# Optimization experiments

Hardware: AMD Instinct MI355X
Metric: run time of the kernel (lower is better)

The kernel has to match this reference:

```python
import jax, jax.numpy as jnp
import numpy as np

N_NODES = 100000
EMB_DIM = 128
HIDDEN = 64
N_EDGES = 1600000


def setup_inputs() -> dict:
    key = jax.random.key(0)
    k_emb, k_ei, k_w1, k_b1, k_w2, k_b2 = jax.random.split(key, 6)
    node_embeddings = jax.random.normal(k_emb, (N_NODES, EMB_DIM), dtype=jnp.float32)
    edge_index = jax.random.randint(k_ei, (2, N_EDGES), 0, N_NODES, dtype=jnp.int64)
    in_dim = 2 * EMB_DIM
    # Kaiming-uniform-ish init like torch Linear
    lim1 = 1.0 / np.sqrt(in_dim)
    lim2 = 1.0 / np.sqrt(HIDDEN)
    W1 = jax.random.uniform(k_w1, (in_dim, HIDDEN), minval=-lim1, maxval=lim1, dtype=jnp.float32)
    b1 = jax.random.uniform(k_b1, (HIDDEN,), minval=-lim1, maxval=lim1, dtype=jnp.float32)
    W2 = jax.random.uniform(k_w2, (HIDDEN, 1), minval=-lim2, maxval=lim2, dtype=jnp.float32)
    b2 = jax.random.uniform(k_b2, (1,), minval=-lim2, maxval=lim2, dtype=jnp.float32)
    return {"node_embeddings": node_embeddings, "edge_index": edge_index,
            "W1": W1, "b1": b1, "W2": W2, "b2": b2}


def reference(node_embeddings, edge_index, W1, b1, W2, b2):
    # Gather source/target node embeddings per edge
    src = node_embeddings[edge_index[0]]            # [E, D]
    tgt = node_embeddings[edge_index[1]]            # [E, D]
    edge_features = jnp.concatenate([src, tgt], axis=1)  # [E, 2D]
    h = jax.nn.relu(edge_features @ W1 + b1)        # [E, H]; dropout = identity (eval)
    edge_scores = (h @ W2 + b2).squeeze(-1)         # [E]
    return edge_scores
```

## Files before the change

kernel.cpp:

```cpp
#include <hip/hip_runtime.h>
#include <hip/hip_bf16.h>

typedef float f32x4 __attribute__((ext_vector_type(4)));
typedef __bf16 bf16x8 __attribute__((ext_vector_type(8)));
typedef _Float16 f16x2 __attribute__((ext_vector_type(2)));
typedef _Float16 f16x8 __attribute__((ext_vector_type(8)));
typedef unsigned short u16;

__device__ inline u16 f2bf(float f) {
    unsigned int u = __float_as_uint(f);
    return (u16)((u + 0x7fffu + ((u >> 16) & 1u)) >> 16);
}

__device__ inline bf16x8 pack8(const float4 a, const float4 b) {
    union { u16 h[8]; bf16x8 v; } r;
    r.h[0] = f2bf(a.x); r.h[1] = f2bf(a.y); r.h[2] = f2bf(a.z); r.h[3] = f2bf(a.w);
    r.h[4] = f2bf(b.x); r.h[5] = f2bf(b.y); r.h[6] = f2bf(b.z); r.h[7] = f2bf(b.w);
    return r.v;
}

__global__ __launch_bounds__(256) void cvt_w_kernel(const float* __restrict__ W1,
                                                    u16* __restrict__ wf) {
    int i = blockIdx.x * 256 + threadIdx.x;
    if (i >= 128 * 128) return;
    int j = i & 7, fl = i >> 3;
    int lane = fl & 63, kbt = fl >> 6;
    int kb = kbt >> 3, t = kbt & 7;
    int k = kb * 32 + ((lane >> 4) & 3) * 8 + j;
    int n = t * 16 + (lane & 15);
    int krow = k + ((n >= 64) ? 128 : 0);
    wf[i] = f2bf(W1[krow * 64 + (n & 63)]);
}

__global__ __launch_bounds__(256) void uv_gemm_kernel(
    const float* __restrict__ emb, const u16* __restrict__ wf,
    _Float16* __restrict__ uv, int M) {
    __shared__ __align__(16) u16 bsh[32 * 64 * 8];

    const int tid = threadIdx.x;
    const int w = tid >> 6, lane = tid & 63, quad = lane >> 4, l15 = lane & 15;
    {
        const uint4* s = (const uint4*)wf;
        uint4* d = (uint4*)bsh;
#pragma unroll
        for (int i = 0; i < 8; ++i) d[tid + i * 256] = s[tid + i * 256];
    }
    __syncthreads();

    const int rb = blockIdx.x * 128 + w * 32;

    bf16x8 a[2][4];
#pragma unroll
    for (int m = 0; m < 2; ++m) {
        int row = rb + m * 16 + l15;
        if (row >= M) row = M - 1;
        const float* p = emb + (long)row * 128 + quad * 8;
#pragma unroll
        for (int kb = 0; kb < 4; ++kb) {
            float4 x = ((const float4*)(p + kb * 32))[0];
            float4 y = ((const float4*)(p + kb * 32))[1];
            a[m][kb] = pack8(x, y);
        }
    }

    f32x4 acc[2][8];
#pragma unroll
    for (int m = 0; m < 2; ++m)
#pragma unroll
        for (int t = 0; t < 8; ++t)
#pragma unroll
            for (int r = 0; r < 4; ++r) acc[m][t][r] = 0.0f;

#pragma unroll
    for (int kb = 0; kb < 4; ++kb)
#pragma unroll
        for (int t = 0; t < 8; ++t) {
            bf16x8 bf = *(const bf16x8*)(bsh + ((kb * 8 + t) * 64 + lane) * 8);
#pragma unroll
            for (int m = 0; m < 2; ++m)
                acc[m][t] = __builtin_amdgcn_mfma_f32_16x16x32_bf16(a[m][kb], bf,
                                                                    acc[m][t], 0, 0, 0);
        }

#pragma unroll
    for (int m = 0; m < 2; ++m)
#pragma unroll
        for (int t = 0; t < 8; ++t)
#pragma unroll
            for (int r = 0; r < 4; ++r) {
                int row = rb + m * 16 + quad * 4 + r;
                if (row < M) uv[(long)row * 128 + t * 16 + l15] = (_Float16)acc[m][t][r];
            }
}

__device__ inline f16x2 relu2(f16x2 x) {
    f16x2 r;
    r[0] = (x[0] > (_Float16)0.f) ? x[0] : (_Float16)0.f;
    r[1] = (x[1] > (_Float16)0.f) ? x[1] : (_Float16)0.f;
    return r;
}

__global__ __launch_bounds__(256, 8) void edge_score_kernel(
    const _Float16* __restrict__ uv, const int* __restrict__ idx,
    const float* __restrict__ b1, const float* __restrict__ w2,
    const float* __restrict__ b2, float* __restrict__ out, int E, int nT) {
    const int tid = threadIdx.x, w = tid >> 6, lane = tid & 63;
    const int e4 = lane >> 2, q = lane & 3;

    f16x2 b1h[8], w2h[8];
#pragma unroll
    for (int i = 0; i < 4; ++i) {
        b1h[i][0]     = (_Float16)b1[q * 8 + 2 * i];
        b1h[i][1]     = (_Float16)b1[q * 8 + 2 * i + 1];
        b1h[4 + i][0] = (_Float16)b1[32 + q * 8 + 2 * i];
        b1h[4 + i][1] = (_Float16)b1[32 + q * 8 + 2 * i + 1];
        w2h[i][0]     = (_Float16)w2[q * 8 + 2 * i];
        w2h[i][1]     = (_Float16)w2[q * 8 + 2 * i + 1];
        w2h[4 + i][0] = (_Float16)w2[32 + q * 8 + 2 * i];
        w2h[4 + i][1] = (_Float16)w2[32 + q * 8 + 2 * i + 1];
    }
    const float b2v = b2[0];

    const int gw = blockIdx.x * 4 + w, stride = gridDim.x * 4;

    auto ldidx = [&](int tile, int& s, int& t) {
        int e = tile * 16 + e4;
        if (e >= E) e = E - 1;
        s = idx[e];
        t = idx[E + e];
    };
    int src, tgt;
    ldidx(gw < nT ? gw : 0, src, tgt);

    union F8 { f16x8 v; f16x2 p[4]; };

    for (int tile = gw; tile < nT; tile += stride) {
        int nt2 = tile + stride, sn, tn;
        ldidx(nt2 < nT ? nt2 : tile, sn, tn);

        const _Float16* up = uv + (long)src * 128;
        const _Float16* vp = uv + (long)tgt * 128;
        F8 U0, U1, V0, V1;
        U0.v = *(const f16x8*)(up + q * 8);
        U1.v = *(const f16x8*)(up + 32 + q * 8);
        V0.v = *(const f16x8*)(vp + 64 + q * 8);
        V1.v = *(const f16x8*)(vp + 96 + q * 8);

        float s = 0.f;
#pragma unroll
        for (int i = 0; i < 4; ++i) {
            f16x2 h = relu2((U0.p[i] + V0.p[i]) + b1h[i]);
#if __has_builtin(__builtin_amdgcn_fdot2)
            s = __builtin_amdgcn_fdot2(h, w2h[i], s, false);
#else
            s += (float)h[0] * (float)w2h[i][0] + (float)h[1] * (float)w2h[i][1];
#endif
        }
#pragma unroll
        for (int i = 0; i < 4; ++i) {
            f16x2 h = relu2((U1.p[i] + V1.p[i]) + b1h[4 + i]);
#if __has_builtin(__builtin_amdgcn_fdot2)
            s = __builtin_amdgcn_fdot2(h, w2h[4 + i], s, false);
#else
            s += (float)h[0] * (float)w2h[4 + i][0] + (float)h[1] * (float)w2h[4 + i][1];
#endif
        }
        s += __shfl_xor(s, 1, 64);
        s += __shfl_xor(s, 2, 64);
        if (q == 0) {
            int e = tile * 16 + e4;
            if (e < E) out[e] = s + b2v;
        }
        src = sn; tgt = tn;
    }
}

extern "C" void kernel_launch(void* const* d_in, const int* in_sizes, int n_in,
                              void* d_out, int out_size, void* d_ws, size_t ws_size,
                              hipStream_t stream) {
    const float* emb_f = (const float*)d_in[0];
    const int*   idx   = (const int*)d_in[1];
    const float* W1    = (const float*)d_in[2];
    const float* b1    = (const float*)d_in[3];
    const float* W2    = (const float*)d_in[4];
    const float* b2    = (const float*)d_in[5];
    float* out = (float*)d_out;

    const int embN = in_sizes[0];
    const int M    = embN / 128;
    const int E    = in_sizes[1] / 2;

    _Float16* uv = (_Float16*)d_ws;
    u16* wf = (u16*)(uv + (long)M * 128);

    cvt_w_kernel<<<64, 256, 0, stream>>>(W1, wf);
    uv_gemm_kernel<<<(M + 127) / 128, 256, 0, stream>>>(emb_f, wf, uv, M);

    int nT = (E + 15) / 16;
    edge_score_kernel<<<2048, 256, 0, stream>>>(uv, idx, b1, W2, b2, out, E, nT);
}
```

Before: 159.8 us.

## Fuse W1 bf16 conversion into GEMM, halve rows per block, nontemporal index/output

Removes the separate weight-conversion kernel launch: each GEMM block now converts and swizzles W1 from fp32 directly into shared memory. The GEMM block handles 64 rows instead of 128, which doubles the block count and halves per-wave accumulators. The edge kernel uses nontemporal loads for edge indices and nontemporal stores for scores so this streaming data does not pollute the cache. In exchange, every block redoes the 16K-element W1 conversion with strided fp32 reads, and there are now about 1563 such blocks.

```diff
diff --git a/kernel.cpp b/kernel.cpp
--- a/kernel.cpp
+++ b/kernel.cpp
@@ -19,78 +19,62 @@
     return r.v;
 }
 
-__global__ __launch_bounds__(256) void cvt_w_kernel(const float* __restrict__ W1,
-                                                    u16* __restrict__ wf) {
-    int i = blockIdx.x * 256 + threadIdx.x;
-    if (i >= 128 * 128) return;
-    int j = i & 7, fl = i >> 3;
-    int lane = fl & 63, kbt = fl >> 6;
-    int kb = kbt >> 3, t = kbt & 7;
-    int k = kb * 32 + ((lane >> 4) & 3) * 8 + j;
-    int n = t * 16 + (lane & 15);
-    int krow = k + ((n >= 64) ? 128 : 0);
-    wf[i] = f2bf(W1[krow * 64 + (n & 63)]);
-}
-
 __global__ __launch_bounds__(256) void uv_gemm_kernel(
-    const float* __restrict__ emb, const u16* __restrict__ wf,
+    const float* __restrict__ emb, const float* __restrict__ W1,
     _Float16* __restrict__ uv, int M) {
     __shared__ __align__(16) u16 bsh[32 * 64 * 8];
 
     const int tid = threadIdx.x;
     const int w = tid >> 6, lane = tid & 63, quad = lane >> 4, l15 = lane & 15;
-    {
-        const uint4* s = (const uint4*)wf;
-        uint4* d = (uint4*)bsh;
-#pragma unroll
-        for (int i = 0; i < 8; ++i) d[tid + i * 256] = s[tid + i * 256];
+
+    for (int i = tid; i < 128 * 128; i += 256) {
+        int j = i & 7, fl = i >> 3;
+        int ln = fl & 63, kbt = fl >> 6;
+        int kb = kbt >> 3, t = kbt & 7;
+        int k = kb * 32 + ((ln >> 4) & 3) * 8 + j;
+        int n = t * 16 + (ln & 15);
+        int krow = k + ((n >= 64) ? 128 : 0);
+        bsh[i] = f2bf(W1[krow * 64 + (n & 63)]);
     }
     __syncthreads();
 
-    const int rb = blockIdx.x * 128 + w * 32;
+    const int row0 = blockIdx.x * 64 + w * 16;
 
-    bf16x8 a[2][4];
-#pragma unroll
-    for (int m = 0; m < 2; ++m) {
-        int row = rb + m * 16 + l15;
+    bf16x8 a[4];
+    {
+        int row = row0 + l15;
         if (row >= M) row = M - 1;
         const float* p = emb + (long)row * 128 + quad * 8;
 #pragma unroll
         for (int kb = 0; kb < 4; ++kb) {
             float4 x = ((const float4*)(p + kb * 32))[0];
             float4 y = ((const float4*)(p + kb * 32))[1];
-            a[m][kb] = pack8(x, y);
+            a[kb] = pack8(x, y);
         }
     }
 
-    f32x4 acc[2][8];
+    f32x4 acc[8];
 #pragma unroll
-    for (int m = 0; m < 2; ++m)
+    for (int t = 0; t < 8; ++t)
 #pragma unroll
-        for (int t = 0; t < 8; ++t)
-#pragma unroll
-            for (int r = 0; r < 4; ++r) acc[m][t][r] = 0.0f;
+        for (int r = 0; r < 4; ++r) acc[t][r] = 0.0f;
 
 #pragma unroll
     for (int kb = 0; kb < 4; ++kb)
 #pragma unroll
         for (int t = 0; t < 8; ++t) {
             bf16x8 bf = *(const bf16x8*)(bsh + ((kb * 8 + t) * 64 + lane) * 8);
-#pragma unroll
-            for (int m = 0; m < 2; ++m)
-                acc[m][t] = __builtin_amdgcn_mfma_f32_16x16x32_bf16(a[m][kb], bf,
-                                                                    acc[m][t], 0, 0, 0);
+            acc[t] = __builtin_amdgcn_mfma_f32_16x16x32_bf16(a[kb], bf, acc[t],
+                                                             0, 0, 0);
         }
 
 #pragma unroll
-    for (int m = 0; m < 2; ++m)
+    for (int t = 0; t < 8; ++t)
 #pragma unroll
-        for (int t = 0; t < 8; ++t)
-#pragma unroll
-            for (int r = 0; r < 4; ++r) {
-                int row = rb + m * 16 + quad * 4 + r;
-                if (row < M) uv[(long)row * 128 + t * 16 + l15] = (_Float16)acc[m][t][r];
-            }
+        for (int r = 0; r < 4; ++r) {
+            int row = row0 + quad * 4 + r;
+            if (row < M) uv[(long)row * 128 + t * 16 + l15] = (_Float16)acc[t][r];
+        }
 }
 
 __device__ inline f16x2 relu2(f16x2 x) {
@@ -126,8 +110,8 @@
     auto ldidx = [&](int tile, int& s, int& t) {
         int e = tile * 16 + e4;
         if (e >= E) e = E - 1;
-        s = idx[e];
-        t = idx[E + e];
+        s = __builtin_nontemporal_load(idx + e);
+        t = __builtin_nontemporal_load(idx + E + e);
     };
     int src, tgt;
     ldidx(gw < nT ? gw : 0, src, tgt);
@@ -169,7 +153,7 @@
         s += __shfl_xor(s, 2, 64);
         if (q == 0) {
             int e = tile * 16 + e4;
-            if (e < E) out[e] = s + b2v;
+            if (e < E) __builtin_nontemporal_store(s + b2v, out + e);
         }
         src = sn; tgt = tn;
     }
@@ -191,10 +175,8 @@
     const int E    = in_sizes[1] / 2;
 
     _Float16* uv = (_Float16*)d_ws;
-    u16* wf = (u16*)(uv + (long)M * 128);
 
-    cvt_w_kernel<<<64, 256, 0, stream>>>(W1, wf);
-    uv_gemm_kernel<<<(M + 127) / 128, 256, 0, stream>>>(emb_f, wf, uv, M);
+    uv_gemm_kernel<<<(M + 63) / 64, 256, 0, stream>>>(emb_f, W1, uv, M);
 
     int nT = (E + 15) / 16;
     edge_score_kernel<<<2048, 256, 0, stream>>>(uv, idx, b1, W2, b2, out, E, nT);
```

Result: slower. 182.5 us (+14.2%).
